# Performance work log

Hardware: AMD Instinct MI355X
Metric: run time of the kernel (lower is better)

## Reference

```python
import jax, jax.numpy as jnp
import numpy as np
from jax import lax

B, CI, CO, H, W = 2, 256, 256, 128, 128
K = 3
K2 = K * K  # 9 kernel taps
BN_EPS = 1e-5


def setup_inputs() -> dict:
    key = jax.random.key(0)
    ks = jax.random.split(key, 9)
    x = jax.random.normal(ks[0], (B, CI, H, W), jnp.float32)
    # conv_offset_mask: Conv2d(chi, 3*K2, 3, stride=1, pad=1) -> [o_y/o_x interleaved (2*K2) | mask (K2)]
    w_off = jax.random.normal(ks[1], (3 * K2, CI, K, K), jnp.float32) * 0.01
    b_off = jax.random.normal(ks[2], (3 * K2,), jnp.float32) * 0.01
    # modulated deformable conv weight/bias
    w_dcn = jax.random.normal(ks[3], (CO, CI, K, K), jnp.float32) * (1.0 / np.float32(np.sqrt(CI * K2)))
    b_dcn = jax.random.normal(ks[4], (CO,), jnp.float32) * 0.01
    # BatchNorm2d (eval-mode affine + running stats)
    gamma = jax.random.uniform(ks[5], (CO,), jnp.float32, 0.5, 1.5)
    beta = jax.random.normal(ks[6], (CO,), jnp.float32) * 0.1
    run_mean = jax.random.normal(ks[7], (CO,), jnp.float32) * 0.1
    run_var = jax.random.uniform(ks[8], (CO,), jnp.float32, 0.5, 1.5)
    return {"x": x, "w_off": w_off, "b_off": b_off, "w_dcn": w_dcn,
            "b_dcn": b_dcn, "gamma": gamma, "beta": beta,
            "run_mean": run_mean, "run_var": run_var}


def _bilinear(x, py, px):
    """Sample x [B,C,H,W] at fractional coords (py,px) [B,H,W]; zero outside."""
    Bx, C, Hx, Wx = x.shape
    y0 = jnp.floor(py)
    x0 = jnp.floor(px)
    ly = py - y0
    lx = px - x0
    xf = x.reshape(Bx, C, Hx * Wx)

    def gather(yy, xx):
        valid = ((yy >= 0) & (yy <= Hx - 1) & (xx >= 0) & (xx <= Wx - 1)).astype(x.dtype)
        yi = jnp.clip(yy, 0, Hx - 1).astype(jnp.int32)
        xi = jnp.clip(xx, 0, Wx - 1).astype(jnp.int32)
        idx = (yi * Wx + xi).reshape(Bx, 1, Hx * Wx)
        v = jnp.take_along_axis(xf, idx, axis=2).reshape(Bx, C, Hx, Wx)
        return v * valid[:, None]

    w00 = ((1 - ly) * (1 - lx))[:, None]
    w01 = ((1 - ly) * lx)[:, None]
    w10 = (ly * (1 - lx))[:, None]
    w11 = (ly * lx)[:, None]
    return (w00 * gather(y0, x0) + w01 * gather(y0, x0 + 1)
            + w10 * gather(y0 + 1, x0) + w11 * gather(y0 + 1, x0 + 1))


def _deform_conv_bn_relu(x, w_off, b_off, w_dcn, b_dcn, gamma, beta, run_mean, run_var):
    # offset/mask predictor conv (stride 1, pad 1)
    om = lax.conv_general_dilated(x, w_off, (1, 1), ((1, 1), (1, 1))) + b_off[None, :, None, None]
    dy = om[:, 0:2 * K2:2]          # [B,K2,H,W]
    dx = om[:, 1:2 * K2:2]          # [B,K2,H,W]
    mask = jax.nn.sigmoid(om[:, 2 * K2:])  # [B,K2,H,W] modulation

    hh = jnp.arange(H, dtype=x.dtype)[:, None]  # [H,1]
    ww = jnp.arange(W, dtype=x.dtype)[None, :]  # [1,W]

    out = jnp.zeros((x.shape[0], w_dcn.shape[0], H, W), x.dtype)
    for k in range(K2):  # fixed small loop over the 9 kernel taps
        i, j = k // K, k % K
        py = hh - 1 + i + dy[:, k]  # pad=1, dilation=1
        px = ww - 1 + j + dx[:, k]
        val = _bilinear(x, py, px) * mask[:, k][:, None]  # [B,CI,H,W]
        out = out + jnp.einsum('oc,bchw->bohw', w_dcn[:, :, i, j], val)
    out = out + b_dcn[None, :, None, None]

    # BatchNorm2d (eval mode) + ReLU
    inv = gamma / jnp.sqrt(run_var + BN_EPS)
    out = out * inv[None, :, None, None] + (beta - run_mean * inv)[None, :, None, None]
    return jnp.maximum(out, 0.0)


def reference(x, w_off, b_off, w_dcn, b_dcn, gamma, beta, run_mean, run_var):
    return _deform_conv_bn_relu(x, w_off, b_off, w_dcn, b_dcn, gamma, beta, run_mean, run_var)
```

## Files before the change

### kernel.cpp

```cpp
#include <hip/hip_runtime.h>
#include <math.h>

#define Bn 2
#define CIc 256
#define COc 256
#define Hh 128
#define Ww 128
#define HW (Hh*Ww)

typedef unsigned short u16;
typedef unsigned int u32;
typedef __bf16 bf16x8 __attribute__((ext_vector_type(8)));
typedef float  f32x4  __attribute__((ext_vector_type(4)));
typedef float  f32x2  __attribute__((ext_vector_type(2)));
typedef u32    u32x4v __attribute__((ext_vector_type(4)));

#define WOFP_OFF  0
#define WPACK_OFF 36864
#define SCALE_OFF 331776
#define SHIFT_OFF 332032
#define XT_OFF    332288

__device__ __forceinline__ u16 f2bf(float f) {
    u32 u = __builtin_bit_cast(u32, f);
    return (u16)((u + 0x7FFFu + ((u >> 16) & 1u)) >> 16);
}
__device__ __forceinline__ u32 pkbf(float lo, float hi) {
    __bf16 a = (__bf16)lo, b = (__bf16)hi;
    return (u32)__builtin_bit_cast(u16, a) | ((u32)__builtin_bit_cast(u16, b) << 16);
}
__device__ __forceinline__ f32x2 unpk(u32 u) {
    f32x2 r;
    r.x = __builtin_bit_cast(float, u << 16);
    r.y = __builtin_bit_cast(float, u & 0xFFFF0000u);
    return r;
}

__global__ void prep_kernel(const float* __restrict__ w_off,
                            const float* __restrict__ w_dcn,
                            const float* __restrict__ b_dcn,
                            const float* __restrict__ gamma,
                            const float* __restrict__ beta,
                            const float* __restrict__ rmean,
                            const float* __restrict__ rvar,
                            float* __restrict__ ws) {
    int tid = blockIdx.x*blockDim.x + threadIdx.x;
    int nth = gridDim.x*blockDim.x;
    u16* wofp = (u16*)(ws + WOFP_OFF);
    u16* wpk  = (u16*)(ws + WPACK_OFF);
    for (int idx = tid; idx < 9*8*32*4*8; idx += nth) {
        int j = idx & 7, kb = (idx>>3)&3, co = (idx>>5)&31, s = (idx>>10)&7, k = idx>>13;
        int ci = kb*64 + s*8 + j;
        float v = (co < 27) ? w_off[(co*CIc + ci)*9 + k] : 0.f;
        wofp[idx] = f2bf(v);
    }
    for (int idx = tid; idx < 9*8*256*4*8; idx += nth) {
        int j = idx & 7, kb = (idx>>3)&3, co = (idx>>5)&255, s = (idx>>13)&7, k = idx>>16;
        int ci = kb*64 + s*8 + j;
        wpk[idx] = f2bf(w_dcn[(co*CIc + ci)*9 + k]);
    }
    if (tid < COc) {
        float inv = gamma[tid] * rsqrtf(rvar[tid] + 1e-5f);
        ws[SCALE_OFF+tid] = inv;
        ws[SHIFT_OFF+tid] = beta[tid] - rmean[tid]*inv + b_dcn[tid]*inv;
    }
}

__global__ __launch_bounds__(256) void transpose_kernel(const float* __restrict__ x,
                                                        float* __restrict__ ws) {
    __shared__ float tile[256][33];
    int bid = blockIdx.x;
    int b   = bid >> 9;
    int pxt = bid & 511;
    const float* xb = x + (size_t)b*CIc*HW + pxt*32;
    int px = threadIdx.x & 31, cg = threadIdx.x >> 5;
    #pragma unroll 8
    for (int it = 0; it < 32; it++) {
        int ci = it*8 + cg;
        tile[ci][px] = xb[(size_t)ci*HW + px];
    }
    __syncthreads();
    int px2 = threadIdx.x >> 3, oct = threadIdx.x & 7;
    u16* xto = (u16*)(ws + XT_OFF) + (((size_t)b*HW + pxt*32 + px2) << 8);
    #pragma unroll
    for (int uu = 0; uu < 4; uu++) {
        int u = uu*8 + oct;
        int cib = (u & 3)*64 + (u >> 2)*8;
        u32x4v v;
        #pragma unroll
        for (int t = 0; t < 4; t++)
            v[t] = pkbf(tile[cib + 2*t][px2], tile[cib + 2*t + 1][px2]);
        *(u32x4v*)(xto + u*8) = v;
    }
}

__device__ __forceinline__ void calc_corners(const float* spy, const float* spxs, const float* smk,
        int k, int p_s, int sub, const u16* xt,
        float& w00, float& w01, float& w10, float& w11,
        const u16*& x00, const u16*& x01, const u16*& x10, const u16*& x11) {
    float pyv = spy[k*64 + p_s], pxv = spxs[k*64 + p_s], mv = smk[k*64 + p_s];
    float y0f = floorf(pyv), x0f = floorf(pxv);
    float ly = pyv - y0f, lx = pxv - x0f;
    int y0 = (int)y0f, x0i = (int)x0f;
    int y1 = y0 + 1, x1i = x0i + 1;
    float wy0 = ((unsigned)y0  < Hh) ? (1.f-ly) : 0.f;
    float wy1 = ((unsigned)y1  < Hh) ? ly       : 0.f;
    float wx0 = ((unsigned)x0i < Ww) ? (1.f-lx) : 0.f;
    float wx1 = ((unsigned)x1i < Ww) ? lx       : 0.f;
    w00 = wy0*wx0*mv; w01 = wy0*wx1*mv; w10 = wy1*wx0*mv; w11 = wy1*wx1*mv;
    int cy0 = min(max(y0,0),Hh-1), cy1 = min(max(y1,0),Hh-1);
    int cx0 = min(max(x0i,0),Ww-1), cx1 = min(max(x1i,0),Ww-1);
    x00 = xt + ((((cy0<<7)+cx0)<<8) + sub*8);
    x01 = xt + ((((cy0<<7)+cx1)<<8) + sub*8);
    x10 = xt + ((((cy1<<7)+cx0)<<8) + sub*8);
    x11 = xt + ((((cy1<<7)+cx1)<<8) + sub*8);
}

#define LOADG(gg, ubase) \
    _Pragma("unroll") for (int t = 0; t < 2; t++) { \
        int o = ((ubase) + t) << 5; \
        gg[t][0] = *(const u32x4v*)(x00 + o); \
        gg[t][1] = *(const u32x4v*)(x01 + o); \
        gg[t][2] = *(const u32x4v*)(x10 + o); \
        gg[t][3] = *(const u32x4v*)(x11 + o); \
    }

#define CONSG(gg, ubase, dst) \
    _Pragma("unroll") for (int t = 0; t < 2; t++) { \
        u32x4v vv; \
        _Pragma("unroll") for (int w2 = 0; w2 < 4; w2++) { \
            f32x2 r = unpk(gg[t][0][w2])*w00 + unpk(gg[t][1][w2])*w01 \
                    + unpk(gg[t][2][w2])*w10 + unpk(gg[t][3][w2])*w11; \
            vv[w2] = pkbf(r.x, r.y); \
        } \
        u32 uoff = (((u32)((ubase) + t) << 6) | wsub) ^ wswz; \
        *(u32x4v*)((dst) + wrbase0 + uoff) = vv; \
    }

#define GEMMSTEP(s) { \
    _Pragma("unroll") for (int bq = 0; bq < 4; bq++) { \
        _Pragma("unroll") for (int mi = 0; mi < 4; mi++) \
            acc[mi][bq] = __builtin_amdgcn_mfma_f32_16x16x32_bf16(apre[(s)&1][mi], bpre[(s)&1][bq], acc[mi][bq], 0,0,0); \
    } }

#define APREF(s, ptr) { \
    _Pragma("unroll") for (int mi = 0; mi < 4; mi++) \
        apre[(s)&1][mi] = *(const bf16x8*)((ptr) + mi*512); }

#define BPREF(sn) { \
    u32 inn = ((u32)((sn)*64 + kb*16)) ^ rswz; \
    _Pragma("unroll") for (int bq = 0; bq < 4; bq++) \
        bpre[(sn)&1][bq] = *(const bf16x8*)(base_r + (pxl + bq*16)*512 + inn); }

__global__ __launch_bounds__(256, 2) void fused_kernel(const float* __restrict__ b_off,
                                                       const float* __restrict__ ws,
                                                       float* __restrict__ out) {
    __shared__ __align__(16) char smem[65536 + 3*576*4];
    float* finA = (float*)(smem + 36864);
    float* spy  = (float*)(smem + 65536);
    float* spxs = spy + 576;
    float* smk  = spxs + 576;

    int tid = threadIdx.x;
    int bid = blockIdx.x;
    int tile = (bid & 7)*64 + (bid >> 3);
    int b = tile >> 8;
    int pixbase = (tile & 255) * 64;
    int h  = pixbase >> 7;
    int w0 = pixbase & 127;

    const u16* wofp = (const u16*)(ws + WOFP_OFF);
    const u16* wpk  = (const u16*)(ws + WPACK_OFF);
    const u16* xt   = (const u16*)(ws + XT_OFF) + (size_t)b*HW*256;

    int l  = tid & 63;
    int wv = tid >> 6;
    int kb = l >> 4;
    int pxl = l & 15;
    int aoff = pxl*32 + kb*8;

    {
        int pxa = wv*16 + pxl;
        f32x4 oa0 = {0.f,0.f,0.f,0.f}, oa1 = {0.f,0.f,0.f,0.f};
        for (int ky = 0; ky < 3; ky++) {
            int y = h + ky - 1;
            if ((unsigned)y < Hh) {
                __syncthreads();
                const u16* xrow = xt + (((size_t)y << 7) << 8);
                for (int c = tid; c < 66*32; c += 256) {
                    int rr = c >> 5, slot = c & 31;
                    int xw = w0 - 1 + rr;
                    u32x4v v = {};
                    if ((unsigned)xw < Ww) v = *(const u32x4v*)(xrow + ((size_t)xw << 8) + slot*8);
                    u32 off = ((u32)(rr*512 + slot*16)) ^ (((u32)(rr & 7)) << 4);
                    *(u32x4v*)(smem + off) = v;
                }
                __syncthreads();
                #pragma unroll
                for (int kx = 0; kx < 3; kx++) {
                    int k = ky*3 + kx;
                    const u16* wk = wofp + k*8192;
                    int rr = pxa + kx;
                    u32 rbase = (u32)rr * 512;
                    u32 rsw = ((u32)(rr & 7)) << 4;
                    #pragma unroll
                    for (int s = 0; s < 8; s++) {
                        u32 off = (rbase + (u32)((s*4 + kb)*16)) ^ rsw;
                        bf16x8 bf = *(const bf16x8*)(smem + off);
                        bf16x8 a0 = *(const bf16x8*)(wk + s*1024 + aoff);
                        bf16x8 a1 = *(const bf16x8*)(wk + s*1024 + 512 + aoff);
                        oa0 = __builtin_amdgcn_mfma_f32_16x16x32_bf16(a0, bf, oa0, 0,0,0);
                        oa1 = __builtin_amdgcn_mfma_f32_16x16x32_bf16(a1, bf, oa1, 0,0,0);
                    }
                }
            }
        }
        __syncthreads();
        #pragma unroll
        for (int r = 0; r < 4; r++) {
            finA[(kb*4 + r)*64 + pxa]      = oa0[r];
            finA[(16 + kb*4 + r)*64 + pxa] = oa1[r];
        }
    }
    __syncthreads();
    for (int idx = tid; idx < 576; idx += 256) {
        int k = idx >> 6, p = idx & 63;
        float dy = finA[(2*k)*64 + p]   + b_off[2*k];
        float dx = finA[(2*k+1)*64 + p] + b_off[2*k+1];
        float mv = finA[(18+k)*64 + p]  + b_off[18+k];
        spy[idx]  = (float)(h - 1 + k/3) + dy;
        spxs[idx] = (float)(w0 + p - 1 + k%3) + dx;
        smk[idx]  = 1.f/(1.f + __expf(-mv));
    }
    __syncthreads();

    int p_s = tid >> 2;
    int sub = tid & 3;
    u32 wrbase0 = (u32)p_s*512;
    u32 wsub = (u32)sub << 4;
    u32 wswz = (u32)(p_s & 7) << 4;
    u32 rswz = (u32)(pxl & 7) << 4;

    f32x4 acc[4][4];
    #pragma unroll
    for (int mi = 0; mi < 4; mi++)
        #pragma unroll
        for (int bq = 0; bq < 4; bq++)
            acc[mi][bq] = (f32x4){0.f,0.f,0.f,0.f};

    bf16x8 apre[2][4];
    bf16x8 bpre[2][4];

    {
        float w00,w01,w10,w11; const u16 *x00,*x01,*x10,*x11;
        calc_corners(spy, spxs, smk, 0, p_s, sub, xt, w00,w01,w10,w11, x00,x01,x10,x11);
        u32x4v ga[2][4], gb[2][4];
        LOADG(ga, 0); LOADG(gb, 2);
        CONSG(ga, 0, smem); CONSG(gb, 2, smem);
        LOADG(ga, 4); LOADG(gb, 6);
        CONSG(ga, 4, smem); CONSG(gb, 6, smem);
    }
    {
        const u16* ap0 = wpk + wv*2048 + aoff;
        #pragma unroll
        for (int mi = 0; mi < 4; mi++) {
            apre[0][mi] = *(const bf16x8*)(ap0 + mi*512);
            apre[1][mi] = *(const bf16x8*)(ap0 + 8192 + mi*512);
        }
    }
    __syncthreads();

    for (int k = 0; k < 8; k++) {
        const char* base_r = smem + ((k & 1) << 15);
        char* base_w = smem + (((k + 1) & 1) << 15);
        const u16* wkb   = wpk + k*65536 + wv*2048 + aoff;
        const u16* wkb_n = wkb + 65536;

        float w00,w01,w10,w11; const u16 *x00,*x01,*x10,*x11;
        calc_corners(spy, spxs, smk, k+1, p_s, sub, xt, w00,w01,w10,w11, x00,x01,x10,x11);

        BPREF(0);

        u32x4v g0[2][4], g1[2][4];
        #pragma unroll
        for (int s = 0; s < 8; s++) {
            __builtin_amdgcn_sched_barrier(0);
            __builtin_amdgcn_s_setprio(1);
            GEMMSTEP(s);
            __builtin_amdgcn_s_setprio(0);
            { const u16* ap = (s < 6) ? (wkb + (s+2)*8192) : (wkb_n + (s-6)*8192); APREF(s, ap); }
            if (s < 7) { BPREF(s+1); }
            if (s == 0) { LOADG(g0, 0); }
            if (s == 1) { LOADG(g1, 2); }
            if (s == 4) { CONSG(g0, 0, base_w); LOADG(g0, 4); }
            if (s == 5) { CONSG(g1, 2, base_w); LOADG(g1, 6); }
            if (s == 7) { CONSG(g0, 4, base_w); }
        }
        CONSG(g1, 6, base_w);
        __syncthreads();
    }
    {
        const char* base_r = smem;
        const u16* wkb = wpk + 8*65536 + wv*2048 + aoff;
        BPREF(0);
        #pragma unroll
        for (int s = 0; s < 8; s++) {
            __builtin_amdgcn_sched_barrier(0);
            __builtin_amdgcn_s_setprio(1);
            GEMMSTEP(s);
            __builtin_amdgcn_s_setprio(0);
            if (s < 6) { const u16* ap = wkb + (s+2)*8192; APREF(s, ap); }
            if (s < 7) { BPREF(s+1); }
        }
    }

    int rbase = kb*4;
    #pragma unroll
    for (int mi = 0; mi < 4; mi++) {
        #pragma unroll
        for (int r = 0; r < 4; r++) {
            int co = wv*64 + mi*16 + rbase + r;
            float sc = ws[SCALE_OFF+co], sh = ws[SHIFT_OFF+co];
            float* op = out + ((size_t)(b*COc + co))*HW + pixbase + pxl;
            #pragma unroll
            for (int bq = 0; bq < 4; bq++)
                op[bq*16] = fmaxf(acc[mi][bq][r]*sc + sh, 0.f);
        }
    }
}

extern "C" void kernel_launch(void* const* d_in, const int* in_sizes, int n_in,
                              void* d_out, int out_size, void* d_ws, size_t ws_size,
                              hipStream_t stream) {
    const float* x     = (const float*)d_in[0];
    const float* w_off = (const float*)d_in[1];
    const float* b_off = (const float*)d_in[2];
    const float* w_dcn = (const float*)d_in[3];
    const float* b_dcn = (const float*)d_in[4];
    const float* gamma = (const float*)d_in[5];
    const float* beta  = (const float*)d_in[6];
    const float* rmean = (const float*)d_in[7];
    const float* rvar  = (const float*)d_in[8];
    float* out = (float*)d_out;
    float* ws  = (float*)d_ws;

    prep_kernel<<<512, 256, 0, stream>>>(w_off, w_dcn, b_dcn, gamma, beta, rmean, rvar, ws);
    transpose_kernel<<<1024, 256, 0, stream>>>(x, ws);
    fused_kernel<<<512, 256, 0, stream>>>(b_off, ws, out);
}
```

Before: 100.1 us.

## Single-buffer the gathered B tile to fit three blocks per CU

Drops the double-buffered shared-memory B tile and the B-fragment register prefetch. Each GEMM step now reads its B operand straight from LDS, and the gather/construct of the next tap runs after a barrier instead of overlapping the MFMAs. Shared memory falls to about 48KB and launch bounds rise to 3 blocks per CU, trading intra-block overlap for more resident waves to hide latency. This adds an extra __syncthreads per tap and serializes the bilinear gather with the compute.

```diff
diff --git a/kernel.cpp b/kernel.cpp
--- a/kernel.cpp
+++ b/kernel.cpp
@@ -138,26 +138,23 @@
     }
 
 #define GEMMSTEP(s) { \
+    u32 inn = ((u32)((s)*64 + kb*16)) ^ rswz; \
     _Pragma("unroll") for (int bq = 0; bq < 4; bq++) { \
+        bf16x8 bb = *(const bf16x8*)(smem + (pxl + bq*16)*512 + inn); \
         _Pragma("unroll") for (int mi = 0; mi < 4; mi++) \
-            acc[mi][bq] = __builtin_amdgcn_mfma_f32_16x16x32_bf16(apre[(s)&1][mi], bpre[(s)&1][bq], acc[mi][bq], 0,0,0); \
+            acc[mi][bq] = __builtin_amdgcn_mfma_f32_16x16x32_bf16(apre[(s)&1][mi], bb, acc[mi][bq], 0,0,0); \
     } }
 
 #define APREF(s, ptr) { \
     _Pragma("unroll") for (int mi = 0; mi < 4; mi++) \
         apre[(s)&1][mi] = *(const bf16x8*)((ptr) + mi*512); }
 
-#define BPREF(sn) { \
-    u32 inn = ((u32)((sn)*64 + kb*16)) ^ rswz; \
-    _Pragma("unroll") for (int bq = 0; bq < 4; bq++) \
-        bpre[(sn)&1][bq] = *(const bf16x8*)(base_r + (pxl + bq*16)*512 + inn); }
-
-__global__ __launch_bounds__(256, 2) void fused_kernel(const float* __restrict__ b_off,
+__global__ __launch_bounds__(256, 3) void fused_kernel(const float* __restrict__ b_off,
                                                        const float* __restrict__ ws,
                                                        float* __restrict__ out) {
-    __shared__ __align__(16) char smem[65536 + 3*576*4];
-    float* finA = (float*)(smem + 36864);
-    float* spy  = (float*)(smem + 65536);
+    __shared__ __align__(16) char smem[48896];
+    float* finA = (float*)(smem + 33792);
+    float* spy  = (float*)(smem + 41984);
     float* spxs = spy + 576;
     float* smk  = spxs + 576;
 
@@ -249,16 +246,16 @@
             acc[mi][bq] = (f32x4){0.f,0.f,0.f,0.f};
 
     bf16x8 apre[2][4];
-    bf16x8 bpre[2][4];
+    u32x4v gc[2][4];
 
     {
         float w00,w01,w10,w11; const u16 *x00,*x01,*x10,*x11;
         calc_corners(spy, spxs, smk, 0, p_s, sub, xt, w00,w01,w10,w11, x00,x01,x10,x11);
-        u32x4v ga[2][4], gb[2][4];
-        LOADG(ga, 0); LOADG(gb, 2);
-        CONSG(ga, 0, smem); CONSG(gb, 2, smem);
-        LOADG(ga, 4); LOADG(gb, 6);
-        CONSG(ga, 4, smem); CONSG(gb, 6, smem);
+        LOADG(gc, 0);
+        CONSG(gc, 0, smem); LOADG(gc, 2);
+        CONSG(gc, 2, smem); LOADG(gc, 4);
+        CONSG(gc, 4, smem); LOADG(gc, 6);
+        CONSG(gc, 6, smem);
     }
     {
         const u16* ap0 = wpk + wv*2048 + aoff;
@@ -271,17 +268,12 @@
     __syncthreads();
 
     for (int k = 0; k < 8; k++) {
-        const char* base_r = smem + ((k & 1) << 15);
-        char* base_w = smem + (((k + 1) & 1) << 15);
         const u16* wkb   = wpk + k*65536 + wv*2048 + aoff;
         const u16* wkb_n = wkb + 65536;
 
         float w00,w01,w10,w11; const u16 *x00,*x01,*x10,*x11;
         calc_corners(spy, spxs, smk, k+1, p_s, sub, xt, w00,w01,w10,w11, x00,x01,x10,x11);
 
-        BPREF(0);
-
-        u32x4v g0[2][4], g1[2][4];
         #pragma unroll
         for (int s = 0; s < 8; s++) {
             __builtin_amdgcn_sched_barrier(0);
@@ -289,20 +281,17 @@
             GEMMSTEP(s);
             __builtin_amdgcn_s_setprio(0);
             { const u16* ap = (s < 6) ? (wkb + (s+2)*8192) : (wkb_n + (s-6)*8192); APREF(s, ap); }
-            if (s < 7) { BPREF(s+1); }
-            if (s == 0) { LOADG(g0, 0); }
-            if (s == 1) { LOADG(g1, 2); }
-            if (s == 4) { CONSG(g0, 0, base_w); LOADG(g0, 4); }
-            if (s == 5) { CONSG(g1, 2, base_w); LOADG(g1, 6); }
-            if (s == 7) { CONSG(g0, 4, base_w); }
-        }
-        CONSG(g1, 6, base_w);
+            if (s == 4) { LOADG(gc, 0); }
+        }
         __syncthreads();
+        CONSG(gc, 0, smem); LOADG(gc, 2);
+        CONSG(gc, 2, smem); LOADG(gc, 4);
+        CONSG(gc, 4, smem); LOADG(gc, 6);
+        CONSG(gc, 6, smem);
+        __syncthreads();
     }
     {
-        const char* base_r = smem;
         const u16* wkb = wpk + 8*65536 + wv*2048 + aoff;
-        BPREF(0);
         #pragma unroll
         for (int s = 0; s < 8; s++) {
             __builtin_amdgcn_sched_barrier(0);
@@ -310,7 +299,6 @@
             GEMMSTEP(s);
             __builtin_amdgcn_s_setprio(0);
             if (s < 6) { const u16* ap = wkb + (s+2)*8192; APREF(s, ap); }
-            if (s < 7) { BPREF(s+1); }
         }
     }
 
```

Measured after the change: 109.7 us. 1.1x slower.
